# Kernel optimization log

Measured on AMD Instinct MI355X. Metric: run time of the kernel, lower is better.

The kernel has to match this reference:

```python
import jax, jax.numpy as jnp
import numpy as np

EPS_WN = 1e-6
EPS_BN = 1e-5

def wn_linear(x, W):
    # WeightNormlinear with scale=False, bias=False: y = (x W^T) / ||W_row||
    norm = jnp.sqrt(jnp.sum(W * W, axis=1) + EPS_WN)  # [out]
    return (x @ W.T) / norm

def hyper_weights(z, W0, W2, W3):
    # z: [N_O, N_I, E] -> conv weight [N_O*16, N_I*16, 3, 3], bias [N_O*16]
    N_O, N_I, E = z.shape
    bias = wn_linear(z.reshape(N_O, N_I * E), W0).reshape(-1)      # [N_O*16]
    w = wn_linear(z, W2).reshape(N_O, N_I, 16, E)                  # fc2
    w = wn_linear(w, W3)                                           # fc3 -> [N_O,N_I,16,16*9]
    w = w.reshape(N_O, N_I, 16, 16, 3, 3).transpose(0, 2, 1, 3, 4, 5)
    w = w.reshape(N_O * 16, N_I * 16, 3, 3)
    return jnp.sign(w), jnp.sign(bias)  # BinarizeWF forward

def conv3x3(x, w, stride):
    return jax.lax.conv_general_dilated(
        x, w, (stride, stride), ((1, 1), (1, 1)),
        dimension_numbers=('NCHW', 'OIHW', 'NCHW'))

def batchnorm(x, gamma, beta):
    # training-mode BN: biased batch statistics over (N,H,W)
    mean = jnp.mean(x, axis=(0, 2, 3), keepdims=True)
    var = jnp.var(x, axis=(0, 2, 3), keepdims=True)
    return gamma[None, :, None, None] * (x - mean) * jax.lax.rsqrt(var + EPS_BN) + beta[None, :, None, None]

def setup_inputs() -> dict:
    key = jax.random.key(0)
    ks = jax.random.split(key, 10)
    B, C, H, W = 16, 256, 56, 56
    E = 64
    NO = NI = C // 16
    def uni(k, shape, s):
        return jax.random.uniform(k, shape, jnp.float32, -s, s)
    stdv_z = 5.0 / np.sqrt(E)          # random_z init
    stdv0 = 4.0 / np.sqrt(E * NI)      # fc0: in = E*N_I
    stdv23 = 4.0 / np.sqrt(E)          # fc2/fc3: in = E
    return {
        'x': jax.random.normal(ks[0], (B, C, H, W), jnp.float32),
        'z1': uni(ks[1], (NO, NI, E), stdv_z),
        'W0_1': uni(ks[2], (16, E * NI), stdv0),
        'W2_1': uni(ks[3], (16 * E, E), stdv23),
        'W3_1': uni(ks[4], (16 * 9, E), stdv23),
        'gamma1': jnp.ones((C,), jnp.float32),
        'beta1': jnp.zeros((C,), jnp.float32),
        'z2': uni(ks[5], (NO, NO, E), stdv_z),
        'W0_2': uni(ks[6], (16, E * NO), stdv0),
        'W2_2': uni(ks[7], (16 * E, E), stdv23),
        'W3_2': uni(ks[8], (16 * 9, E), stdv23),
        'gamma2': jnp.ones((C,), jnp.float32),
        'beta2': jnp.zeros((C,), jnp.float32),
    }

def reference(x, z1, W0_1, W2_1, W3_1, gamma1, beta1,
              z2, W0_2, W2_2, W3_2, gamma2, beta2):
    residual = x
    # conv1 (stride=1): binarize activations (C != 3), hyper-generated binary weights
    w1, b1 = hyper_weights(z1, W0_1, W2_1, W3_1)
    out = conv3x3(jnp.sign(x), w1, 1) + b1[None, :, None, None]
    out = batchnorm(out, gamma1, beta1)
    # conv2
    w2, b2 = hyper_weights(z2, W0_2, W2_2, W3_2)
    out2 = conv3x3(jnp.sign(out), w2, 1) + b2[None, :, None, None]
    out2 = batchnorm(out2, gamma2, beta2)
    return out2 + residual
```

## Files before the change

### kernel.cpp

```cpp
#include <hip/hip_runtime.h>
#include <stdint.h>

typedef int v4i __attribute__((ext_vector_type(4)));
typedef int v16i __attribute__((ext_vector_type(16)));



__global__ __launch_bounds__(256, 2) void fused_pre_kernel(
    const float* __restrict__ z1, const float* __restrict__ W21,
    const float* __restrict__ W31, const float* __restrict__ z2,
    const float* __restrict__ W22, const float* __restrict__ W32,
    int8_t* __restrict__ Wb1, int8_t* __restrict__ Wb2,
    const float* __restrict__ W01, const float* __restrict__ W02,
    int* __restrict__ b1, int* __restrict__ b2,
    unsigned long long* __restrict__ sums,
    const float* __restrict__ x, int8_t* __restrict__ Sp) {
  __shared__ __align__(16) float Wt[16384];
  __shared__ __align__(16) float hbuf[1024];
  __shared__ __align__(16) float zsh[64];
  __shared__ __align__(16) int8_t pk[2304];
  const int tid = threadIdx.x;

  if (blockIdx.x >= 545) {
    const int fs = blockIdx.x - 545;
    const int xcd = blockIdx.x & 7;
    const int orig = xcd * 116 + (fs >> 3);
    const int b = orig / 58, h = orig % 58;
    int8_t* rowp = Sp + ((size_t)b * 58 + h) * 58 * 256;
    if (h == 0 || h == 57) {
      #pragma unroll
      for (int i = 0; i < 4; ++i) {
        int idx = i * 256 + tid;
        if (idx < 928) *(v4i*)(rowp + (size_t)idx * 16) = (v4i){0, 0, 0, 0};
      }
      return;
    }
    int8_t* t = (int8_t*)Wt;
    const float* xb = x + (size_t)b * 802816 + (size_t)(h - 1) * 56;
    for (int i = 0; i < 56; ++i) {
      int flat = i * 256 + tid;
      int c = flat / 56, w = flat - c * 56;
      float v = xb[(size_t)c * 3136 + w];
      t[w * 256 + (c ^ ((w & 31) << 3))] = (v > 0.f) ? 1 : ((v < 0.f) ? -1 : 0);
    }
    if (tid < 32) {
      int col = tid >> 4;
      *(v4i*)(rowp + (col ? 57 * 256 : 0) + (tid & 15) * 16) = (v4i){0, 0, 0, 0};
    }
    __syncthreads();
    int8_t* dst = rowp + 256;
    for (int i = 0; i < 7; ++i) {
      int f8 = i * 256 + tid;
      int w = f8 >> 5, c0 = (f8 & 31) << 3;
      uint2 v = *(const uint2*)&t[w * 256 + (c0 ^ ((w & 31) << 3))];
      *(uint2*)(dst + (size_t)w * 256 + c0) = v;
    }
    return;
  }

  if (blockIdx.x >= 512) {
    const int pb = blockIdx.x - 512;
    if (pb == 32) {
      #pragma unroll
      for (int i = 0; i < 4; ++i) sums[i * 256 + tid] = 0ull;
      return;
    }
    float* zs = Wt;
    const int set = pb >> 4, o = pb & 15;
    const float* z = set ? z2 : z1;
    const float* W0 = set ? W02 : W01;
    int* bout = set ? b2 : b1;
    #pragma unroll
    for (int i = 0; i < 4; ++i) zs[i * 256 + tid] = z[(size_t)o * 1024 + i * 256 + tid];
    __syncthreads();
    const int j = tid >> 4, l = tid & 15;
    const float* wr = W0 + (size_t)j * 1024;
    double acc = 0.0;
    #pragma unroll 4
    for (int it = 0; it < 16; ++it) {
      float4 w4 = *(const float4*)&wr[it * 64 + l * 4];
      float4 z4 = *(const float4*)&zs[it * 64 + l * 4];
      acc += (double)w4.x * z4.x + (double)w4.y * z4.y + (double)w4.z * z4.z + (double)w4.w * z4.w;
    }
    #pragma unroll
    for (int m = 1; m < 16; m <<= 1) acc += __shfl_xor(acc, m, 64);
    if (l == 0) bout[o * 16 + j] = (acc > 0.0) ? 1 : ((acc < 0.0) ? -1 : 0);
    return;
  }

  const int set = blockIdx.x >> 8;
  const int oi = blockIdx.x & 255;
  const float* z = set ? z2 : z1;
  const float* W2 = set ? W22 : W21;
  const float* W3 = set ? W32 : W31;
  int8_t* Wb = set ? Wb2 : Wb1;

  if (tid < 16) *(float4*)&zsh[tid * 4] = ((const float4*)(z + (size_t)oi * 64))[tid];
  __syncthreads();

  for (int c = 0; c < 4; ++c) {
    if (c) __syncthreads();
    const float4* src = (const float4*)W2 + c * 4096;
    #pragma unroll
    for (int i = 0; i < 16; ++i) {
      int G = i * 256 + tid;
      int row = G >> 4, g = G & 15;
      *(float4*)&Wt[row * 64 + ((g ^ (row & 15)) << 2)] = src[G];
    }
    __syncthreads();
    double ax = 0, ay = 0, az = 0, aw = 0;
    double nx = 0, ny = 0, nz = 0, nw = 0;
    #pragma unroll
    for (int it = 0; it < 16; ++it) {
      float4 w4 = *(const float4*)&Wt[tid * 64 + ((it ^ (tid & 15)) << 2)];
      float4 z4 = *(const float4*)&zsh[it * 4];
      ax += (double)w4.x * z4.x; ay += (double)w4.y * z4.y;
      az += (double)w4.z * z4.z; aw += (double)w4.w * z4.w;
      nx += (double)w4.x * w4.x; ny += (double)w4.y * w4.y;
      nz += (double)w4.z * w4.z; nw += (double)w4.w * w4.w;
    }
    double dot = (ax + ay) + (az + aw);
    double ss = (nx + ny) + (nz + nw);
    hbuf[c * 256 + tid] = (float)(dot / sqrt(ss + 1e-6));
  }
  __syncthreads();

  {
    const float4* src = (const float4*)W3;
    #pragma unroll
    for (int i = 0; i < 9; ++i) {
      int G = i * 256 + tid;
      int row = G >> 4, g = G & 15;
      *(float4*)&Wt[row * 64 + ((g ^ (row & 15)) << 2)] = src[G];
    }
  }
  __syncthreads();

  {
    const int q = tid >> 4, sub = tid & 15;
    #pragma unroll
    for (int k = 0; k < 9; ++k) {
      int jj = sub + (k << 4);
      double ax = 0, ay = 0, az = 0, aw = 0;
      #pragma unroll
      for (int it = 0; it < 16; ++it) {
        float4 w4 = *(const float4*)&Wt[jj * 64 + ((it ^ sub) << 2)];
        float4 h4 = *(const float4*)&hbuf[q * 64 + it * 4];
        ax += (double)w4.x * h4.x; ay += (double)w4.y * h4.y;
        az += (double)w4.z * h4.z; aw += (double)w4.w * h4.w;
      }
      double acc = (ax + ay) + (az + aw);
      int8_t sgn = (acc > 0.0) ? (int8_t)1 : ((acc < 0.0) ? (int8_t)(-1) : (int8_t)0);
      int tp = jj / 9, tap = jj - tp * 9;
      pk[tap * 256 + q * 16 + tp] = sgn;
    }
  }
  __syncthreads();

  if (tid < 144) {
    const int tap = tid >> 4, qq = tid & 15;
    const int o = oi >> 4, ii = oi & 15;
    const int chunk = ((tap << 2) + (ii >> 2)) * 2 + ((ii >> 1) & 1);
    v4i val = *(const v4i*)&pk[tap * 256 + qq * 16];
    *(v4i*)(Wb + (size_t)chunk * 8192 + (size_t)(o * 16 + qq) * 32 + ((ii & 1) << 4)) = val;
  }
}


template <int MODE>
__global__ __launch_bounds__(512, 4) void conv_kernel(
    const int8_t* __restrict__ Sp, const int16_t* __restrict__ rawin,
    const unsigned long long* __restrict__ sumsIn,
    const float* __restrict__ gamma, const float* __restrict__ beta,
    const int8_t* __restrict__ WbP, const int* __restrict__ bias,
    int16_t* __restrict__ raw, unsigned long long* __restrict__ sumsOut)
{
  __shared__ __align__(16) int8_t lds[59392];
  __shared__ float thrS[256];
  __shared__ int sfS[256];
  const int tid = threadIdx.x;
  const int lane = tid & 63;
  const int f0 = blockIdx.x + 28 * blockIdx.y;
  const int orig = (f0 & 7) * 56 + (f0 >> 3);
  const int b = orig / 28, bx = orig % 28;
  const int H0 = bx << 1;

  const int n = lane & 31, kg = lane >> 5;
  const int wid = tid >> 6;
  const int cogrp = wid & 3, pxgrp = wid >> 2;

  if (MODE == 1) {
    if (tid < 256) {
      double S = (double)(long long)sumsIn[tid];
      double Q = (double)(long long)sumsIn[256 + tid];
      double mean = S / 50176.0;
      double var = Q / 50176.0 - mean * mean;
      double istd = 1.0 / sqrt(var + 1e-5);
      double A = (double)gamma[tid] * istd;
      float Af = (float)A;
      float thr; int sf;
      if (Af > 0.f)      { thr = (float)(mean - (double)beta[tid] / A); sf = 1; }
      else if (Af < 0.f) { thr = (float)(mean - (double)beta[tid] / A); sf = -1; }
      else               { thr = -1e30f; sf = (beta[tid] > 0.f) ? 1 : ((beta[tid] < 0.f) ? -1 : 0); }
      thrS[tid] = thr; sfS[tid] = sf;
    }
    __syncthreads();
  }

  const int8_t* Abase = WbP + (size_t)((cogrp << 6) + n) * 32 + (kg << 4);
  v4i Ar[2][2][2];
  #pragma unroll
  for (int c2 = 0; c2 < 2; ++c2)
    #pragma unroll
    for (int a = 0; a < 2; ++a)
      Ar[0][c2][a] = *(const v4i*)(Abase + (size_t)c2 * 8192 + a * 1024);

  if (MODE == 0) {
    const int8_t* SpB = Sp + ((size_t)b * 58 + H0) * 58 * 256;
    #pragma unroll
    for (int ph = 0; ph < 2; ++ph) {
      v4i tmp[4];
      #pragma unroll
      for (int it = 0; it < 4; ++it) {
        int G = (ph * 4 + it) * 512 + tid;
        if (G < 3712) {
          int pp = G >> 4, gl = G & 15;
          int wp = pp % 58;
          tmp[it] = *(const v4i*)(SpB + pp * 256 + ((gl ^ (wp & 7)) << 4));
        }
      }
      #pragma unroll
      for (int it = 0; it < 4; ++it) {
        int G = (ph * 4 + it) * 512 + tid;
        if (G < 3712) *(v4i*)(lds + (G << 4)) = tmp[it];
      }
    }
  } else {
    const int gsrc = tid & 15;
    const int ppt = tid >> 4;
    float thr[16]; int sf[16];
    #pragma unroll
    for (int j = 0; j < 16; ++j) { thr[j] = thrS[gsrc * 16 + j]; sf[j] = sfS[gsrc * 16 + j]; }
    #pragma unroll
    for (int it = 0; it < 8; ++it) {
      int pp = it * 32 + ppt;
      if (pp < 232) {
        int prow = pp / 58, pcol = pp - prow * 58;
        int ir = H0 + prow - 1, ic = pcol - 1;
        v4i outv = (v4i){0, 0, 0, 0};
        if (ir >= 0 && ir <= 55 && ic >= 0 && ic <= 55) {
          const int16_t* src = rawin + ((size_t)(b * 3136 + ir * 56 + ic)) * 256 + gsrc * 16;
          v4i lo = *(const v4i*)src;
          v4i hi = *(const v4i*)(src + 8);
          #pragma unroll
          for (int j = 0; j < 16; ++j) {
            int wd = (j < 8) ? lo[(j >> 1) & 3] : hi[(j >> 1) & 3];
            int v = (j & 1) ? (wd >> 16) : (int)(short)wd;
            float fv = (float)v;
            int bj = (fv > thr[j]) ? sf[j] : ((fv < thr[j]) ? -sf[j] : 0);
            outv[j >> 2] |= (bj & 0xff) << ((j & 3) << 3);
          }
        }
        *(v4i*)(lds + ((pp << 4) + (gsrc ^ (pcol & 7))) * 16) = outv;
      }
    }
  }

  int pixoff[2], wcol[2];
  #pragma unroll
  for (int f = 0; f < 2; ++f) {
    int px = (((pxgrp << 1) + f) << 5) + n;
    if (px > 111) px = 111;
    int hh = px / 56, ww = px - hh * 56;
    pixoff[f] = hh * 58 + ww;
    wcol[f] = ww;
  }

  v16i acc[2][2];
  #pragma unroll
  for (int f = 0; f < 2; ++f)
    #pragma unroll
    for (int a = 0; a < 2; ++a)
      #pragma unroll
      for (int e = 0; e < 16; ++e) acc[f][a][e] = 0;

  __syncthreads();

  #pragma unroll
  for (int ks = 0; ks < 36; ++ks) {
    const int cur = ks & 1;
    if (ks + 1 < 36) {
      #pragma unroll
      for (int c2 = 0; c2 < 2; ++c2)
        #pragma unroll
        for (int a = 0; a < 2; ++a)
          Ar[cur ^ 1][c2][a] = *(const v4i*)(Abase + (size_t)((ks + 1) * 2 + c2) * 8192 + a * 1024);
    }
    const int tap = ks >> 2, c64 = ks & 3;
    const int r = tap / 3, s = tap - 3 * (tap / 3);
    #pragma unroll
    for (int c2 = 0; c2 < 2; ++c2) {
      v4i Af0 = Ar[cur][c2][0], Af1 = Ar[cur][c2][1];
      #pragma unroll
      for (int f = 0; f < 2; ++f) {
        const int gb = (c64 << 2) + (c2 << 1) + kg;
        v4i Bf = *(const v4i*)(lds + ((pixoff[f] + r * 58 + s) << 8)
                               + ((gb ^ ((wcol[f] + s) & 7)) << 4));
        acc[f][0] = __builtin_amdgcn_mfma_i32_32x32x32_i8(Af0, Bf, acc[f][0], 0, 0, 0);
        acc[f][1] = __builtin_amdgcn_mfma_i32_32x32x32_i8(Af1, Bf, acc[f][1], 0, 0, 0);
      }
    }
  }

  __syncthreads();
  #pragma unroll
  for (int f = 0; f < 2; ++f) {
    int px = (((pxgrp << 1) + f) << 5) + n;
    if (px < 112) {
      #pragma unroll
      for (int a = 0; a < 2; ++a) {
        #pragma unroll
        for (int q = 0; q < 4; ++q) {
          int co = (cogrp << 6) + (a << 5) + (q << 3) + (kg << 2);
          v4i bi = *(const v4i*)(bias + co);
          short4 o;
          o.x = (short)(acc[f][a][q * 4 + 0] + bi.x);
          o.y = (short)(acc[f][a][q * 4 + 1] + bi.y);
          o.z = (short)(acc[f][a][q * 4 + 2] + bi.z);
          o.w = (short)(acc[f][a][q * 4 + 3] + bi.w);
          int g = co >> 3;
          *(short4*)(lds + px * 512 + ((g ^ (px & 31)) << 4) + (kg << 3)) = o;
        }
      }
    }
  }
  __syncthreads();
  const int pbase = b * 3136 + bx * 112;
  const int gg = tid & 31;
  int s8[8], q8[8];
  #pragma unroll
  for (int j = 0; j < 8; ++j) { s8[j] = 0; q8[j] = 0; }
  #pragma unroll
  for (int i = 0; i < 7; ++i) {
    int rrow = i * 16 + (tid >> 5);
    v4i val = *(const v4i*)(lds + rrow * 512 + ((gg ^ (rrow & 31)) << 4));
    *(v4i*)(raw + (size_t)(pbase + rrow) * 256 + gg * 8) = val;
    #pragma unroll
    for (int j = 0; j < 8; ++j) {
      int wd = val[j >> 1];
      int v = (j & 1) ? (wd >> 16) : (int)(short)wd;
      s8[j] += v; q8[j] += v * v;
    }
  }
  __syncthreads();
  int* red = (int*)lds;
  #pragma unroll
  for (int j = 0; j < 8; ++j) { red[tid * 8 + j] = s8[j]; red[4096 + tid * 8 + j] = q8[j]; }
  __syncthreads();
  if (tid < 256) {
    const int ch = tid;
    const int own = ch >> 3, sub = ch & 7;
    long long S = 0, Q = 0;
    #pragma unroll
    for (int jj = 0; jj < 16; ++jj) {
      int t2 = own + 32 * jj;
      S += red[t2 * 8 + sub];
      Q += red[4096 + t2 * 8 + sub];
    }
    atomicAdd(&sumsOut[ch], (unsigned long long)S);
    atomicAdd(&sumsOut[256 + ch], (unsigned long long)Q);
  }
}


__global__ void final_kernel(const int16_t* __restrict__ raw2,
                             const unsigned long long* __restrict__ sums2,
                             const float* __restrict__ gamma, const float* __restrict__ beta,
                             const float* __restrict__ x, float* __restrict__ out) {
  __shared__ float t[256 * 57];
  __shared__ __align__(16) float mS[256], AS[256], bS[256];
  const int tid = threadIdx.x;
  const int f0 = blockIdx.x + 56 * blockIdx.y;
  const int orig = (f0 & 7) * 112 + (f0 >> 3);
  const int b = orig / 56, h = orig % 56;
  const int rowp = b * 3136 + h * 56;
  {
    double S = (double)(long long)sums2[tid];
    double Q = (double)(long long)sums2[256 + tid];
    double mean = S / 50176.0;
    double var = Q / 50176.0 - mean * mean;
    double istd = 1.0 / sqrt(var + 1e-5);
    mS[tid] = (float)mean;
    AS[tid] = gamma[tid] * (float)istd;
    bS[tid] = beta[tid];
  }
  __syncthreads();
  for (int i = 0; i < 7; ++i) {
    int f8 = i * 256 + tid;
    int px = f8 >> 5, c0 = (f8 & 31) << 3;
    float m[8], A[8], bb[8];
    *(float4*)&m[0]  = *(const float4*)&mS[c0];
    *(float4*)&m[4]  = *(const float4*)&mS[c0 + 4];
    *(float4*)&A[0]  = *(const float4*)&AS[c0];
    *(float4*)&A[4]  = *(const float4*)&AS[c0 + 4];
    *(float4*)&bb[0] = *(const float4*)&bS[c0];
    *(float4*)&bb[4] = *(const float4*)&bS[c0 + 4];
    v4i vv = *(const v4i*)(raw2 + (size_t)(rowp + px) * 256 + c0);
    #pragma unroll
    for (int j = 0; j < 8; ++j) {
      int wd = vv[j >> 1];
      int v = (j & 1) ? (wd >> 16) : (int)(short)wd;
      t[(c0 + j) * 57 + px] = ((float)v - m[j]) * A[j] + bb[j];
    }
  }
  __syncthreads();
  const float* xb = x + (size_t)b * 802816 + (size_t)h * 56;
  float* ob = out + (size_t)b * 802816 + (size_t)h * 56;
  for (int i = 0; i < 16; ++i) {
    int idx = i * 256 + tid;
    int c = idx >> 4, wq = idx & 15;
    if (wq < 14) {
      int w0 = wq * 4;
      float4 xv = *(const float4*)(xb + (size_t)c * 3136 + w0);
      float4 o;
      o.x = t[c * 57 + w0 + 0] + xv.x;
      o.y = t[c * 57 + w0 + 1] + xv.y;
      o.z = t[c * 57 + w0 + 2] + xv.z;
      o.w = t[c * 57 + w0 + 3] + xv.w;
      *(float4*)(ob + (size_t)c * 3136 + w0) = o;
    }
  }
}


extern "C" void kernel_launch(void* const* d_in, const int* in_sizes, int n_in,
                              void* d_out, int out_size, void* d_ws, size_t ws_size,
                              hipStream_t stream) {
  const float* x      = (const float*)d_in[0];
  const float* z1     = (const float*)d_in[1];
  const float* W0_1   = (const float*)d_in[2];
  const float* W2_1   = (const float*)d_in[3];
  const float* W3_1   = (const float*)d_in[4];
  const float* gamma1 = (const float*)d_in[5];
  const float* beta1  = (const float*)d_in[6];
  const float* z2     = (const float*)d_in[7];
  const float* W0_2   = (const float*)d_in[8];
  const float* W2_2   = (const float*)d_in[9];
  const float* W3_2   = (const float*)d_in[10];
  const float* gamma2 = (const float*)d_in[11];
  const float* beta2  = (const float*)d_in[12];
  float* out = (float*)d_out;

  char* ws = (char*)d_ws;
  size_t off = 0;
  auto alloc = [&](size_t sz) -> void* {
    void* p = ws + off;
    off += (sz + 255) & ~(size_t)255;
    return p;
  };
  int8_t* Sp1   = (int8_t*)alloc(13778944);
  int16_t* raw1 = (int16_t*)alloc(25690112);
  int16_t* raw2 = (int16_t*)alloc(25690112);
  int8_t* Wb1   = (int8_t*)alloc(589824);
  int8_t* Wb2   = (int8_t*)alloc(589824);
  int* b1       = (int*)alloc(1024);
  int* b2       = (int*)alloc(1024);
  unsigned long long* sums = (unsigned long long*)alloc(8192);
  if (ws_size < off) return;

  fused_pre_kernel<<<1473, 256, 0, stream>>>(z1, W2_1, W3_1, z2, W2_2, W3_2, Wb1, Wb2,
                                             W0_1, W0_2, b1, b2, sums, x, Sp1);
  conv_kernel<0><<<dim3(28, 16), 512, 0, stream>>>(Sp1, nullptr, nullptr, nullptr, nullptr,
                                                   Wb1, b1, raw1, sums);
  conv_kernel<1><<<dim3(28, 16), 512, 0, stream>>>(nullptr, raw1, sums, gamma1, beta1,
                                                   Wb2, b2, raw2, sums + 512);
  final_kernel<<<dim3(56, 16), 256, 0, stream>>>(raw2, sums + 512, gamma2, beta2, x, out);
}
```

Before: 172.8 us.

## Remap conv warps to 32 channels by all pixels and fix LDS swizzles

The conv kernel's warp tiling changes from 64 channels × 64 pixels per wave to 32 channels × all 128 pixel slots per wave. Each wave now loads one A fragment per k-step instead of two, and the A prefetch is deepened to a 3-slot ring two steps ahead. The cost is that each wave reads four B fragments from LDS per k-step instead of two. Separately, the hypernetwork pre-kernel gets a stronger XOR swizzle and a padded hbuf row stride (72) to reduce LDS bank conflicts.

New measurement: 219.7 us. 1.27x slower.

```diff
diff --git a/kernel.cpp b/kernel.cpp
--- a/kernel.cpp
+++ b/kernel.cpp
@@ -16,7 +16,7 @@
     unsigned long long* __restrict__ sums,
     const float* __restrict__ x, int8_t* __restrict__ Sp) {
   __shared__ __align__(16) float Wt[16384];
-  __shared__ __align__(16) float hbuf[1024];
+  __shared__ __align__(16) float hbuf[16 * 72];
   __shared__ __align__(16) float zsh[64];
   __shared__ __align__(16) int8_t pk[2304];
   const int tid = threadIdx.x;
@@ -98,6 +98,7 @@
   if (tid < 16) *(float4*)&zsh[tid * 4] = ((const float4*)(z + (size_t)oi * 64))[tid];
   __syncthreads();
 
+  const int key2 = (tid ^ (tid >> 4)) & 15;
   for (int c = 0; c < 4; ++c) {
     if (c) __syncthreads();
     const float4* src = (const float4*)W2 + c * 4096;
@@ -105,14 +106,14 @@
     for (int i = 0; i < 16; ++i) {
       int G = i * 256 + tid;
       int row = G >> 4, g = G & 15;
-      *(float4*)&Wt[row * 64 + ((g ^ (row & 15)) << 2)] = src[G];
+      *(float4*)&Wt[row * 64 + (((g ^ row ^ (row >> 4)) & 15) << 2)] = src[G];
     }
     __syncthreads();
     double ax = 0, ay = 0, az = 0, aw = 0;
     double nx = 0, ny = 0, nz = 0, nw = 0;
     #pragma unroll
     for (int it = 0; it < 16; ++it) {
-      float4 w4 = *(const float4*)&Wt[tid * 64 + ((it ^ (tid & 15)) << 2)];
+      float4 w4 = *(const float4*)&Wt[tid * 64 + ((it ^ key2) << 2)];
       float4 z4 = *(const float4*)&zsh[it * 4];
       ax += (double)w4.x * z4.x; ay += (double)w4.y * z4.y;
       az += (double)w4.z * z4.z; aw += (double)w4.w * z4.w;
@@ -121,7 +122,8 @@
     }
     double dot = (ax + ay) + (az + aw);
     double ss = (nx + ny) + (nz + nw);
-    hbuf[c * 256 + tid] = (float)(dot / sqrt(ss + 1e-6));
+    int j = c * 256 + tid;
+    hbuf[(j >> 6) * 72 + (j & 63)] = (float)(dot / sqrt(ss + 1e-6));
   }
   __syncthreads();
 
@@ -131,7 +133,7 @@
     for (int i = 0; i < 9; ++i) {
       int G = i * 256 + tid;
       int row = G >> 4, g = G & 15;
-      *(float4*)&Wt[row * 64 + ((g ^ (row & 15)) << 2)] = src[G];
+      *(float4*)&Wt[row * 64 + (((g ^ row ^ (row >> 4)) & 15) << 2)] = src[G];
     }
   }
   __syncthreads();
@@ -141,11 +143,12 @@
     #pragma unroll
     for (int k = 0; k < 9; ++k) {
       int jj = sub + (k << 4);
+      const int key3 = (sub ^ k) & 15;
       double ax = 0, ay = 0, az = 0, aw = 0;
       #pragma unroll
       for (int it = 0; it < 16; ++it) {
-        float4 w4 = *(const float4*)&Wt[jj * 64 + ((it ^ sub) << 2)];
-        float4 h4 = *(const float4*)&hbuf[q * 64 + it * 4];
+        float4 w4 = *(const float4*)&Wt[jj * 64 + ((it ^ key3) << 2)];
+        float4 h4 = *(const float4*)&hbuf[q * 72 + it * 4];
         ax += (double)w4.x * h4.x; ay += (double)w4.y * h4.y;
         az += (double)w4.z * h4.z; aw += (double)w4.w * h4.w;
       }
@@ -187,7 +190,6 @@
 
   const int n = lane & 31, kg = lane >> 5;
   const int wid = tid >> 6;
-  const int cogrp = wid & 3, pxgrp = wid >> 2;
 
   if (MODE == 1) {
     if (tid < 256) {
@@ -207,13 +209,13 @@
     __syncthreads();
   }
 
-  const int8_t* Abase = WbP + (size_t)((cogrp << 6) + n) * 32 + (kg << 4);
-  v4i Ar[2][2][2];
-  #pragma unroll
-  for (int c2 = 0; c2 < 2; ++c2)
-    #pragma unroll
-    for (int a = 0; a < 2; ++a)
-      Ar[0][c2][a] = *(const v4i*)(Abase + (size_t)c2 * 8192 + a * 1024);
+  const int8_t* Abase = WbP + (size_t)((wid << 5) + n) * 32 + (kg << 4);
+  v4i Ar[3][2];
+  #pragma unroll
+  for (int c2 = 0; c2 < 2; ++c2) {
+    Ar[0][c2] = *(const v4i*)(Abase + (size_t)(0 * 2 + c2) * 8192);
+    Ar[1][c2] = *(const v4i*)(Abase + (size_t)(1 * 2 + c2) * 8192);
+  }
 
   if (MODE == 0) {
     const int8_t* SpB = Sp + ((size_t)b * 58 + H0) * 58 * 256;
@@ -266,71 +268,64 @@
     }
   }
 
-  int pixoff[2], wcol[2];
-  #pragma unroll
-  for (int f = 0; f < 2; ++f) {
-    int px = (((pxgrp << 1) + f) << 5) + n;
+  int pixoff[4], wcol[4];
+  #pragma unroll
+  for (int f = 0; f < 4; ++f) {
+    int px = (f << 5) + n;
     if (px > 111) px = 111;
     int hh = px / 56, ww = px - hh * 56;
     pixoff[f] = hh * 58 + ww;
     wcol[f] = ww;
   }
 
-  v16i acc[2][2];
-  #pragma unroll
-  for (int f = 0; f < 2; ++f)
-    #pragma unroll
-    for (int a = 0; a < 2; ++a)
-      #pragma unroll
-      for (int e = 0; e < 16; ++e) acc[f][a][e] = 0;
+  v16i acc[4];
+  #pragma unroll
+  for (int f = 0; f < 4; ++f)
+    #pragma unroll
+    for (int e = 0; e < 16; ++e) acc[f][e] = 0;
 
   __syncthreads();
 
   #pragma unroll
   for (int ks = 0; ks < 36; ++ks) {
-    const int cur = ks & 1;
-    if (ks + 1 < 36) {
+    const int cur = ks % 3;
+    if (ks + 2 < 36) {
+      const int bn = (ks + 2) % 3;
       #pragma unroll
       for (int c2 = 0; c2 < 2; ++c2)
-        #pragma unroll
-        for (int a = 0; a < 2; ++a)
-          Ar[cur ^ 1][c2][a] = *(const v4i*)(Abase + (size_t)((ks + 1) * 2 + c2) * 8192 + a * 1024);
+        Ar[bn][c2] = *(const v4i*)(Abase + (size_t)((ks + 2) * 2 + c2) * 8192);
     }
     const int tap = ks >> 2, c64 = ks & 3;
     const int r = tap / 3, s = tap - 3 * (tap / 3);
     #pragma unroll
     for (int c2 = 0; c2 < 2; ++c2) {
-      v4i Af0 = Ar[cur][c2][0], Af1 = Ar[cur][c2][1];
-      #pragma unroll
-      for (int f = 0; f < 2; ++f) {
+      v4i Af = Ar[cur][c2];
+      #pragma unroll
+      for (int f = 0; f < 4; ++f) {
         const int gb = (c64 << 2) + (c2 << 1) + kg;
         v4i Bf = *(const v4i*)(lds + ((pixoff[f] + r * 58 + s) << 8)
                                + ((gb ^ ((wcol[f] + s) & 7)) << 4));
-        acc[f][0] = __builtin_amdgcn_mfma_i32_32x32x32_i8(Af0, Bf, acc[f][0], 0, 0, 0);
-        acc[f][1] = __builtin_amdgcn_mfma_i32_32x32x32_i8(Af1, Bf, acc[f][1], 0, 0, 0);
-      }
-    }
-  }
-
-  __syncthreads();
-  #pragma unroll
-  for (int f = 0; f < 2; ++f) {
-    int px = (((pxgrp << 1) + f) << 5) + n;
-    if (px < 112) {
-      #pragma unroll
-      for (int a = 0; a < 2; ++a) {
-        #pragma unroll
-        for (int q = 0; q < 4; ++q) {
-          int co = (cogrp << 6) + (a << 5) + (q << 3) + (kg << 2);
-          v4i bi = *(const v4i*)(bias + co);
-          short4 o;
-          o.x = (short)(acc[f][a][q * 4 + 0] + bi.x);
-          o.y = (short)(acc[f][a][q * 4 + 1] + bi.y);
-          o.z = (short)(acc[f][a][q * 4 + 2] + bi.z);
-          o.w = (short)(acc[f][a][q * 4 + 3] + bi.w);
-          int g = co >> 3;
-          *(short4*)(lds + px * 512 + ((g ^ (px & 31)) << 4) + (kg << 3)) = o;
-        }
+        acc[f] = __builtin_amdgcn_mfma_i32_32x32x32_i8(Af, Bf, acc[f], 0, 0, 0);
+      }
+    }
+  }
+
+  __syncthreads();
+  #pragma unroll
+  for (int f = 0; f < 4; ++f) {
+    int px = (f << 5) + n;
+    if (px < 112 && (f < 3 || n < 16)) {
+      #pragma unroll
+      for (int q = 0; q < 4; ++q) {
+        int co = (wid << 5) + (q << 3) + (kg << 2);
+        v4i bi = *(const v4i*)(bias + co);
+        short4 o;
+        o.x = (short)(acc[f][q * 4 + 0] + bi.x);
+        o.y = (short)(acc[f][q * 4 + 1] + bi.y);
+        o.z = (short)(acc[f][q * 4 + 2] + bi.z);
+        o.w = (short)(acc[f][q * 4 + 3] + bi.w);
+        int g = (wid << 2) + q;
+        *(short4*)(lds + px * 512 + ((g ^ (px & 31)) << 4) + (kg << 3)) = o;
       }
     }
   }
```
